# Kernel optimization log

Measured on AMD Instinct MI355X. Metric: run time of the kernel, lower is better.

## Reference

```python
import jax, jax.numpy as jnp
import numpy as np
from jax import lax

K = 3      # kernel_size
PAD = 1    # padding
OG = 2     # offset groups


def _conv2d(x, w, b):
    y = lax.conv_general_dilated(x, w, (1, 1), [(PAD, PAD), (PAD, PAD)],
                                 dimension_numbers=('NCHW', 'OIHW', 'NCHW'))
    return y + b[None, :, None, None]


def _deform_conv2d(x, offset, mask, weight):
    # torchvision-style modulated deform_conv2d (v2), stride=1, dilation=1,
    # zero out-of-bounds, offset layout [B, OG*K*K*2, H, W] with (dy, dx) pairs.
    B, C, H, W = x.shape
    O = weight.shape[0]
    K2 = K * K
    Cg = C // OG

    ki, kj = jnp.meshgrid(jnp.arange(K), jnp.arange(K), indexing='ij')
    ki = ki.reshape(K2)
    kj = kj.reshape(K2)
    base_y = jnp.arange(H)[None, :] - PAD + ki[:, None]   # [K2, H]
    base_x = jnp.arange(W)[None, :] - PAD + kj[:, None]   # [K2, W]

    off = offset.reshape(B, OG, K2, 2, H, W)
    py = off[:, :, :, 0] + base_y[None, None, :, :, None].astype(x.dtype)  # [B,OG,K2,H,W]
    px = off[:, :, :, 1] + base_x[None, None, :, None, :].astype(x.dtype)
    m = mask.reshape(B, OG, K2, H, W)

    y0f = jnp.floor(py)
    x0f = jnp.floor(px)
    wy1 = py - y0f   # bilinear weights, grads flow through py/px
    wx1 = px - x0f
    y0 = y0f.astype(jnp.int32)
    x0 = x0f.astype(jnp.int32)
    y1 = y0 + 1
    x1 = x0 + 1

    img = x.reshape(B, OG, Cg, H * W)

    def gather(yi, xi):
        valid = (yi >= 0) & (yi < H) & (xi >= 0) & (xi < W)
        idx = jnp.clip(yi, 0, H - 1) * W + jnp.clip(xi, 0, W - 1)          # [B,OG,K2,H,W]
        v = jnp.take_along_axis(img[:, :, :, None, :],
                                idx.reshape(B, OG, 1, K2, H * W), axis=-1)
        return v.reshape(B, OG, Cg, K2, H, W) * valid[:, :, None].astype(x.dtype)

    v00 = gather(y0, x0)
    v01 = gather(y0, x1)
    v10 = gather(y1, x0)
    v11 = gather(y1, x1)

    wy1e = wy1[:, :, None]   # [B,OG,1,K2,H,W]
    wx1e = wx1[:, :, None]
    val = (v00 * (1 - wy1e) * (1 - wx1e)
           + v01 * (1 - wy1e) * wx1e
           + v10 * wy1e * (1 - wx1e)
           + v11 * wy1e * wx1e)
    val = val * m[:, :, None]                               # modulation mask

    wr = weight.reshape(O, OG, Cg, K2)
    return jnp.einsum('ogck,bgckhw->bohw', wr, val)


def setup_inputs() -> dict:
    key = jax.random.key(0)
    k1, k2, k3, k4, k5 = jax.random.split(key, 5)
    B, C, O, H, W = 4, 64, 64, 128, 128
    K2 = K * K
    x = jax.random.normal(k1, (B, C, H, W), dtype=jnp.float32)
    w_main = jax.random.normal(k2, (O, C, K, K), dtype=jnp.float32) / np.sqrt(C * K2)
    w_off = jax.random.normal(k3, (2 * OG * K2, C, K, K), dtype=jnp.float32) * 0.01
    b_off = jax.random.normal(k4, (2 * OG * K2,), dtype=jnp.float32) * 0.01
    w_mask = jnp.full((OG * K2, C, K, K), 0.5, dtype=jnp.float32)  # init_mask = 0.5
    b_mask = jax.random.normal(k5, (OG * K2,), dtype=jnp.float32) * 0.01
    return {"x": x, "w_main": w_main, "w_off": w_off, "b_off": b_off,
            "w_mask": w_mask, "b_mask": b_mask}


def reference(x, w_main, w_off, b_off, w_mask, b_mask):
    offset = _conv2d(x, w_off, b_off)
    mask = jax.nn.sigmoid(_conv2d(x, w_mask, b_mask))
    return _deform_conv2d(x, offset, mask, w_main)
```

## Files before the change

### kernel.cpp

```cpp
#include <hip/hip_runtime.h>
#include <math.h>

#define BB 4
#define C 64
#define O 64
#define H 128
#define W 128
#define K2 9
#define HW (H*W)
#define NOFF 36

typedef __bf16 bf16;
typedef bf16 bf16x8 __attribute__((ext_vector_type(8)));
typedef float f32x4 __attribute__((ext_vector_type(4)));
typedef unsigned short u16x8 __attribute__((ext_vector_type(8)));
typedef unsigned int u32x4 __attribute__((ext_vector_type(4)));

#define BSTR 55
#define B2STR 19
#define VSTR 36
#define SSTR 72
#define VAL_OFF 14688
#define SMEM_BYTES 28512
#define WFRAG 18432
#define NW_TOTAL 73728

__device__ inline unsigned short f2h_bits(float f) {
  _Float16 h = (_Float16)f;
  return __builtin_bit_cast(unsigned short, h);
}
__device__ inline float h2f(unsigned short u) {
  return (float)__builtin_bit_cast(_Float16, u);
}

__global__ __launch_bounds__(256) void prep_all(
    const float* __restrict__ x, const float* __restrict__ w_main,
    const float* __restrict__ w_off, const float* __restrict__ w_mask,
    unsigned short* __restrict__ xT16, bf16* __restrict__ wfC,
    bf16* __restrict__ wfM) {
  __shared__ float tile[64][68];
  int tid = threadIdx.x;
  int b = blockIdx.x >> 8;
  int p0 = (blockIdx.x & 255) * 64;
#pragma unroll
  for (int it = 0; it < 4; ++it) {
    int c = it * 16 + (tid >> 4);
    int p4 = (tid & 15) * 4;
    *(f32x4*)&tile[c][p4] =
        *(const f32x4*)(x + (size_t)(b * C + c) * HW + p0 + p4);
  }
  __syncthreads();
#pragma unroll
  for (int it = 0; it < 2; ++it) {
    int t = it * 256 + tid;
    int p = t >> 3;
    int h8 = t & 7;
    u16x8 o;
#pragma unroll
    for (int j = 0; j < 8; ++j) {
      bf16 v = (bf16)tile[h8 * 8 + j][p];
      o[j] = __builtin_bit_cast(unsigned short, v);
    }
    *(u16x8*)&xT16[(size_t)(b * HW + p0 + p) * C + h8 * 8] = o;
  }
  int i = blockIdx.x * 256 + tid;
  if (i < NW_TOTAL) {
    int which = (i >= 36864);
    int ii = which ? i - 36864 : i;
    int j = ii & 7;
    int l = (ii >> 3) & 63;
    int rest = ii >> 9;
    int to = rest & 3;
    int kk = (rest >> 2) % 9;
    int ph = (rest >> 2) / 9;
    int m = to * 16 + (l & 15);
    int u = kk * 32 + (l >> 4) * 8 + j;
    int tap = u >> 5;
    int c1 = u & 31;
    if (!which) {
      int c = ph * 32 + c1;
      float v = (m < NOFF) ? w_off[(m * C + c) * K2 + tap]
                : (m < 54) ? w_mask[((m - NOFF) * C + c) * K2 + tap]
                           : 0.f;
      wfC[ii] = (bf16)v;
    } else {
      wfM[ii] = (bf16)w_main[(m * C + ph * 32 + c1) * K2 + tap];
    }
  }
}

__global__ __launch_bounds__(256, 5) void fused_deform(
    const bf16* __restrict__ xT, const bf16* __restrict__ wfC,
    const bf16* __restrict__ wfM, const float* __restrict__ b_off,
    const float* __restrict__ b_mask, float* __restrict__ out) {
  __shared__ __align__(16) char smem[SMEM_BYTES];
  bf16* stage = (bf16*)smem;
  float* bufF = (float*)smem;
  u32x4* buf2 = (u32x4*)smem;
  float* valF = (float*)smem;
  bf16* val = (bf16*)(smem + VAL_OFF);

  const int tid = threadIdx.x;
  const int lane = tid & 63;
  const int wv = tid >> 6;
  const int n16 = lane & 15;
  const int q4 = lane >> 4;
  const int nt = wv & 1;
  const int mh = wv >> 1;
  const int row = nt * 16 + n16;
  const int pg = tid >> 3;
  const int ch = tid & 7;

  const int g8 = blockIdx.x & 7;
  const int slot = blockIdx.x >> 3;
  const int b = g8 >> 1;
  const int ti = (g8 & 1) * 256 + slot;
  const int h0 = ti >> 2;
  const int w0 = (ti & 3) * 32;
  const bf16* xb = xT + (size_t)b * HW * C;

  bf16x8 zero8;
#pragma unroll
  for (int j = 0; j < 8; ++j) zero8[j] = (bf16)0.f;

#pragma unroll
  for (int it = 0; it < 4; ++it) {
    int id = it * 256 + tid;
    if (id < 816) {
      int chk = id & 7;
      int rest = id >> 3;
      int wp = rest % 34;
      int r = rest / 34;
      int yy = h0 + r - 1;
      int xx = w0 + wp - 1;
      bf16x8 v = zero8;
      if ((unsigned)yy < (unsigned)H && (unsigned)xx < (unsigned)W)
        v = *(const bf16x8*)(xb + (size_t)((yy << 7) + xx) * C + chk * 8);
      *(bf16x8*)(stage + (r * 34 + wp) * SSTR + chk * 8) = v;
    }
  }
  __syncthreads();
  f32x4 accC[2] = {{0.f,0.f,0.f,0.f},{0.f,0.f,0.f,0.f}};
#pragma unroll 1
  for (int ph = 0; ph < 2; ++ph) {
#pragma unroll
    for (int kk = 0; kk < 9; ++kk) {
      bf16x8 bfr = *(const bf16x8*)(stage +
          ((kk / 3) * 34 + row + kk % 3) * SSTR + ph * 32 + q4 * 8);
#pragma unroll
      for (int i = 0; i < 2; ++i) {
        int to = 2 * mh + i;
        bf16x8 afr = *(const bf16x8*)(wfC +
            (size_t)(((ph * 9 + kk) * 4 + to) * 64 + lane) * 8);
        accC[i] = __builtin_amdgcn_mfma_f32_16x16x32_bf16(afr, bfr, accC[i], 0, 0, 0);
      }
    }
  }
  __syncthreads();

#pragma unroll
  for (int i = 0; i < 2; ++i)
#pragma unroll
    for (int r = 0; r < 4; ++r) {
      int o = (2 * mh + i) * 16 + q4 * 4 + r;
      float a = accC[i][r];
      if (o < NOFF) {
        bufF[row * BSTR + o] = a + b_off[o];
      } else if (o < 54) {
        float s = a + b_mask[o - NOFF];
        bufF[row * BSTR + o] = 1.f / (1.f + __expf(-s));
      }
    }
  __syncthreads();

  unsigned int rW0[3], rW1[3], rCo[3];
#pragma unroll
  for (int it = 0; it < 3; ++it) {
    int t = it * 256 + tid;
    if (t < 576) {
      int p = t & 31;
      int gk = t >> 5;
      int g = gk / 9, tap = gk % 9;
      float offy = bufF[p * BSTR + 2 * gk];
      float offx = bufF[p * BSTR + 2 * gk + 1];
      float m = bufF[p * BSTR + NOFF + gk];
      float py = offy + (float)(h0 + tap / 3 - 1);
      float px = offx + (float)(w0 + p + tap % 3 - 1);
      float y0f = floorf(py), x0f = floorf(px);
      float wy1 = py - y0f, wx1 = px - x0f;
      float wy0 = 1.f - wy1, wx0 = 1.f - wx1;
      int y0 = (int)y0f, x0 = (int)x0f;
      int y1 = y0 + 1, x1 = x0 + 1;
      bool y0ok = (unsigned)y0 < (unsigned)H, y1ok = (unsigned)y1 < (unsigned)H;
      bool x0ok = (unsigned)x0 < (unsigned)W, x1ok = (unsigned)x1 < (unsigned)W;
      float w00 = (y0ok && x0ok) ? wy0 * wx0 * m : 0.f;
      float w01 = (y0ok && x1ok) ? wy0 * wx1 * m : 0.f;
      float w10 = (y1ok && x0ok) ? wy1 * wx0 * m : 0.f;
      float w11 = (y1ok && x1ok) ? wy1 * wx1 * m : 0.f;
      unsigned int y0c = (unsigned)min(max(y0, 0), H - 1);
      unsigned int y1c = (unsigned)min(max(y1, 0), H - 1);
      unsigned int x0c = (unsigned)min(max(x0, 0), W - 1);
      unsigned int x1c = (unsigned)min(max(x1, 0), W - 1);
      rW0[it] = (unsigned)f2h_bits(w00) | ((unsigned)f2h_bits(w01) << 16);
      rW1[it] = (unsigned)f2h_bits(w10) | ((unsigned)f2h_bits(w11) << 16);
      rCo[it] = y0c | (x0c << 8) | (y1c << 16) | (x1c << 24);
    }
  }
  __syncthreads();
#pragma unroll
  for (int it = 0; it < 3; ++it) {
    int t = it * 256 + tid;
    if (t < 576) {
      int p = t & 31;
      int gk = t >> 5;
      u32x4 pk = {rW0[it], rW1[it], rCo[it], 0u};
      buf2[p * B2STR + gk] = pk;
    }
  }
  __syncthreads();

  f32x4 accM[2] = {{0.f,0.f,0.f,0.f},{0.f,0.f,0.f,0.f}};
  const bf16* bb = xb + ch * 8;
  const int gg = ch >> 2;
#pragma unroll 1
  for (int kc = 0; kc < 3; ++kc) {
    if (kc) __syncthreads();
#pragma unroll
    for (int t = 0; t < 3; ++t) {
      int tap = kc * 3 + t;
      u32x4 t4 = buf2[pg * B2STR + gg * 9 + tap];
      float w00 = h2f(t4.x & 0xffff), w01 = h2f(t4.x >> 16);
      float w10 = h2f(t4.y & 0xffff), w11 = h2f(t4.y >> 16);
      int r0 = (int)(t4.z & 255) << 7;
      int x0 = (int)((t4.z >> 8) & 255);
      int r1 = (int)((t4.z >> 16) & 255) << 7;
      int x1 = (int)(t4.z >> 24);
      bf16x8 v00 = *(const bf16x8*)(bb + (size_t)(r0 + x0) * C);
      bf16x8 v01 = *(const bf16x8*)(bb + (size_t)(r0 + x1) * C);
      bf16x8 v10 = *(const bf16x8*)(bb + (size_t)(r1 + x0) * C);
      bf16x8 v11 = *(const bf16x8*)(bb + (size_t)(r1 + x1) * C);
      bf16x8 res;
#pragma unroll
      for (int j = 0; j < 8; ++j) {
        float v = (float)v00[j] * w00 + (float)v01[j] * w01 +
                  (float)v10[j] * w10 + (float)v11[j] * w11;
        res[j] = (bf16)v;
      }
      *(bf16x8*)(val + (t * 32 + pg) * SSTR + ch * 8) = res;
    }
    __syncthreads();
#pragma unroll
    for (int t = 0; t < 3; ++t) {
      int tap = kc * 3 + t;
#pragma unroll
      for (int g = 0; g < 2; ++g) {
        bf16x8 bfr = *(const bf16x8*)(val +
            (t * 32 + row) * SSTR + g * 32 + q4 * 8);
#pragma unroll
        for (int i = 0; i < 2; ++i) {
          int to = 2 * mh + i;
          bf16x8 afr = *(const bf16x8*)(wfM + (size_t)g * WFRAG +
              (size_t)((tap * 4 + to) * 64 + lane) * 8);
          accM[i] = __builtin_amdgcn_mfma_f32_16x16x32_bf16(afr, bfr, accM[i], 0, 0, 0);
        }
      }
    }
  }

  __syncthreads();
#pragma unroll
  for (int i = 0; i < 2; ++i)
#pragma unroll
    for (int r = 0; r < 4; ++r)
      valF[((2 * mh + i) * 16 + q4 * 4 + r) * VSTR + row] = accM[i][r];
  __syncthreads();
  {
    float* ob = out + (size_t)b * O * HW + (h0 << 7) + w0;
#pragma unroll
    for (int it = 0; it < 2; ++it) {
      int id = it * 256 + tid;
      int o = id >> 3, seg = id & 7;
      f32x4 v = *(f32x4*)&valF[o * VSTR + seg * 4];
      *(f32x4*)&ob[(size_t)o * HW + seg * 4] = v;
    }
  }
}

extern "C" void kernel_launch(void* const* d_in, const int* in_sizes, int n_in,
                              void* d_out, int out_size, void* d_ws,
                              size_t ws_size, hipStream_t stream) {
  const float* x = (const float*)d_in[0];
  const float* w_main = (const float*)d_in[1];
  const float* w_off = (const float*)d_in[2];
  const float* b_off = (const float*)d_in[3];
  const float* w_mask = (const float*)d_in[4];
  const float* b_mask = (const float*)d_in[5];
  float* out = (float*)d_out;

  unsigned short* xT16 = (unsigned short*)d_ws;
  bf16* wfC = (bf16*)(xT16 + (size_t)BB * HW * C);
  bf16* wfM = wfC + 36864;

  prep_all<<<1024, 256, 0, stream>>>(x, w_main, w_off, w_mask, xT16, wfC, wfM);
  fused_deform<<<2048, 256, 0, stream>>>((const bf16*)xT16, wfC, wfM, b_off,
                                         b_mask, out);
}
```

Measured before the change: 115.0 us.

## Double pixel tile to 64 per block with 512 threads and remapped wave roles

Each block now covers 64 output pixels of one row using 512 threads, where before it covered 32 pixels with 256 threads. Waves are reassigned so each wave owns one output-channel tile and two pixel tiles, which lets it load a weight fragment once and reuse it across two MFMAs. The wider tile also shrinks the halo overhead of the staged input and the grid shrinks to 1024 blocks. In exchange, shared memory grows to about 46 KB per block, which may reduce occupancy, and the staging and bilinear-value buffers are laid out differently.

Measured after the change: 108.8 us. 1.06x faster.

```diff
diff --git a/kernel.cpp b/kernel.cpp
--- a/kernel.cpp
+++ b/kernel.cpp
@@ -18,10 +18,10 @@
 
 #define BSTR 55
 #define B2STR 19
-#define VSTR 36
+#define VSTR 68
 #define SSTR 72
-#define VAL_OFF 14688
-#define SMEM_BYTES 28512
+#define BUF2_OFF 27648
+#define SMEM_BYTES 47104
 #define WFRAG 18432
 #define NW_TOTAL 73728
 
@@ -89,34 +89,32 @@
   }
 }
 
-__global__ __launch_bounds__(256, 5) void fused_deform(
+__global__ __launch_bounds__(512, 6) void fused_deform(
     const bf16* __restrict__ xT, const bf16* __restrict__ wfC,
     const bf16* __restrict__ wfM, const float* __restrict__ b_off,
     const float* __restrict__ b_mask, float* __restrict__ out) {
   __shared__ __align__(16) char smem[SMEM_BYTES];
   bf16* stage = (bf16*)smem;
   float* bufF = (float*)smem;
-  u32x4* buf2 = (u32x4*)smem;
+  bf16* val = (bf16*)smem;
   float* valF = (float*)smem;
-  bf16* val = (bf16*)(smem + VAL_OFF);
+  u32x4* buf2 = (u32x4*)(smem + BUF2_OFF);
 
   const int tid = threadIdx.x;
   const int lane = tid & 63;
   const int wv = tid >> 6;
   const int n16 = lane & 15;
   const int q4 = lane >> 4;
-  const int nt = wv & 1;
-  const int mh = wv >> 1;
-  const int row = nt * 16 + n16;
+  const int to = wv & 3;
+  const int nh = wv >> 2;
   const int pg = tid >> 3;
   const int ch = tid & 7;
 
   const int g8 = blockIdx.x & 7;
   const int slot = blockIdx.x >> 3;
   const int b = g8 >> 1;
-  const int ti = (g8 & 1) * 256 + slot;
-  const int h0 = ti >> 2;
-  const int w0 = (ti & 3) * 32;
+  const int h0 = slot;
+  const int w0 = (g8 & 1) * 64;
   const bf16* xb = xT + (size_t)b * HW * C;
 
   bf16x8 zero8;
@@ -125,18 +123,18 @@
 
 #pragma unroll
   for (int it = 0; it < 4; ++it) {
-    int id = it * 256 + tid;
-    if (id < 816) {
+    int id = it * 512 + tid;
+    if (id < 1584) {
       int chk = id & 7;
       int rest = id >> 3;
-      int wp = rest % 34;
-      int r = rest / 34;
+      int wp = rest % 66;
+      int r = rest / 66;
       int yy = h0 + r - 1;
       int xx = w0 + wp - 1;
       bf16x8 v = zero8;
       if ((unsigned)yy < (unsigned)H && (unsigned)xx < (unsigned)W)
         v = *(const bf16x8*)(xb + (size_t)((yy << 7) + xx) * C + chk * 8);
-      *(bf16x8*)(stage + (r * 34 + wp) * SSTR + chk * 8) = v;
+      *(bf16x8*)(stage + (r * 66 + wp) * SSTR + chk * 8) = v;
     }
   }
   __syncthreads();
@@ -145,13 +143,13 @@
   for (int ph = 0; ph < 2; ++ph) {
 #pragma unroll
     for (int kk = 0; kk < 9; ++kk) {
-      bf16x8 bfr = *(const bf16x8*)(stage +
-          ((kk / 3) * 34 + row + kk % 3) * SSTR + ph * 32 + q4 * 8);
+      bf16x8 afr = *(const bf16x8*)(wfC +
+          (size_t)(((ph * 9 + kk) * 4 + to) * 64 + lane) * 8);
 #pragma unroll
       for (int i = 0; i < 2; ++i) {
-        int to = 2 * mh + i;
-        bf16x8 afr = *(const bf16x8*)(wfC +
-            (size_t)(((ph * 9 + kk) * 4 + to) * 64 + lane) * 8);
+        int p = (2 * nh + i) * 16 + n16;
+        bf16x8 bfr = *(const bf16x8*)(stage +
+            ((kk / 3) * 66 + p + kk % 3) * SSTR + ph * 32 + q4 * 8);
         accC[i] = __builtin_amdgcn_mfma_f32_16x16x32_bf16(afr, bfr, accC[i], 0, 0, 0);
       }
     }
@@ -162,13 +160,14 @@
   for (int i = 0; i < 2; ++i)
 #pragma unroll
     for (int r = 0; r < 4; ++r) {
-      int o = (2 * mh + i) * 16 + q4 * 4 + r;
+      int o = to * 16 + q4 * 4 + r;
+      int p = (2 * nh + i) * 16 + n16;
       float a = accC[i][r];
       if (o < NOFF) {
-        bufF[row * BSTR + o] = a + b_off[o];
+        bufF[p * BSTR + o] = a + b_off[o];
       } else if (o < 54) {
         float s = a + b_mask[o - NOFF];
-        bufF[row * BSTR + o] = 1.f / (1.f + __expf(-s));
+        bufF[p * BSTR + o] = 1.f / (1.f + __expf(-s));
       }
     }
   __syncthreads();
@@ -176,10 +175,10 @@
   unsigned int rW0[3], rW1[3], rCo[3];
 #pragma unroll
   for (int it = 0; it < 3; ++it) {
-    int t = it * 256 + tid;
-    if (t < 576) {
-      int p = t & 31;
-      int gk = t >> 5;
+    int t = it * 512 + tid;
+    if (t < 1152) {
+      int p = t & 63;
+      int gk = t >> 6;
       int g = gk / 9, tap = gk % 9;
       float offy = bufF[p * BSTR + 2 * gk];
       float offx = bufF[p * BSTR + 2 * gk + 1];
@@ -209,10 +208,10 @@
   __syncthreads();
 #pragma unroll
   for (int it = 0; it < 3; ++it) {
-    int t = it * 256 + tid;
-    if (t < 576) {
-      int p = t & 31;
-      int gk = t >> 5;
+    int t = it * 512 + tid;
+    if (t < 1152) {
+      int p = t & 63;
+      int gk = t >> 6;
       u32x4 pk = {rW0[it], rW1[it], rCo[it], 0u};
       buf2[p * B2STR + gk] = pk;
     }
@@ -246,7 +245,7 @@
                   (float)v10[j] * w10 + (float)v11[j] * w11;
         res[j] = (bf16)v;
       }
-      *(bf16x8*)(val + (t * 32 + pg) * SSTR + ch * 8) = res;
+      *(bf16x8*)(val + (t * 64 + pg) * SSTR + ch * 8) = res;
     }
     __syncthreads();
 #pragma unroll
@@ -254,13 +253,13 @@
       int tap = kc * 3 + t;
 #pragma unroll
       for (int g = 0; g < 2; ++g) {
-        bf16x8 bfr = *(const bf16x8*)(val +
-            (t * 32 + row) * SSTR + g * 32 + q4 * 8);
+        bf16x8 afr = *(const bf16x8*)(wfM + (size_t)g * WFRAG +
+            (size_t)((tap * 4 + to) * 64 + lane) * 8);
 #pragma unroll
         for (int i = 0; i < 2; ++i) {
-          int to = 2 * mh + i;
-          bf16x8 afr = *(const bf16x8*)(wfM + (size_t)g * WFRAG +
-              (size_t)((tap * 4 + to) * 64 + lane) * 8);
+          int p = (2 * nh + i) * 16 + n16;
+          bf16x8 bfr = *(const bf16x8*)(val +
+              (t * 64 + p) * SSTR + g * 32 + q4 * 8);
           accM[i] = __builtin_amdgcn_mfma_f32_16x16x32_bf16(afr, bfr, accM[i], 0, 0, 0);
         }
       }
@@ -272,14 +271,14 @@
   for (int i = 0; i < 2; ++i)
 #pragma unroll
     for (int r = 0; r < 4; ++r)
-      valF[((2 * mh + i) * 16 + q4 * 4 + r) * VSTR + row] = accM[i][r];
+      valF[(to * 16 + q4 * 4 + r) * VSTR + (2 * nh + i) * 16 + n16] = accM[i][r];
   __syncthreads();
   {
     float* ob = out + (size_t)b * O * HW + (h0 << 7) + w0;
 #pragma unroll
     for (int it = 0; it < 2; ++it) {
-      int id = it * 256 + tid;
-      int o = id >> 3, seg = id & 7;
+      int id = it * 512 + tid;
+      int o = id >> 4, seg = id & 15;
       f32x4 v = *(f32x4*)&valF[o * VSTR + seg * 4];
       *(f32x4*)&ob[(size_t)o * HW + seg * 4] = v;
     }
@@ -302,6 +301,6 @@
   bf16* wfM = wfC + 36864;
 
   prep_all<<<1024, 256, 0, stream>>>(x, w_main, w_off, w_mask, xT16, wfC, wfM);
-  fused_deform<<<2048, 256, 0, stream>>>((const bf16*)xT16, wfC, wfM, b_off,
+  fused_deform<<<1024, 512, 0, stream>>>((const bf16*)xT16, wfC, wfM, b_off,
                                          b_mask, out);
 }
```
